# Kernel optimization log

Hardware: AMD Instinct MI355X
Metric: run time of the kernel (lower is better)

## Reference

```python
import jax, jax.numpy as jnp
import numpy as np

# config constants
H = 1024          # hidden_size
I = 512           # moe_intermediate_size
IS = 1024         # moe_shared_expert_intermediate_size
E = 16            # n_routed_experts
G = 4             # n_group
TOPK_G = 2        # topk_group
TOPK = 4          # num_experts_per_tok
SCALE = 2.5       # routed_scaling_factor
B, S = 2, 1024


def _relu2(x):
    r = jax.nn.relu(x)
    return r * r


def setup_inputs() -> dict:
    key = jax.random.key(0)
    ks = jax.random.split(key, 8)
    sd = 0.02
    return {
        "hidden_states": jax.random.normal(ks[0], (B, S, H), jnp.float32),
        "Wg": jax.random.normal(ks[1], (E, H), jnp.float32) * sd,          # router gate weight
        "bias_corr": jax.random.normal(ks[2], (E,), jnp.float32) * 0.01,    # e_score_correction_bias
        "W1": jax.random.normal(ks[3], (E, I, H), jnp.float32) * sd,        # experts up_proj
        "W2": jax.random.normal(ks[4], (E, H, I), jnp.float32) * sd,        # experts down_proj
        "Ws1": jax.random.normal(ks[5], (IS, H), jnp.float32) * sd,         # shared up_proj
        "Ws2": jax.random.normal(ks[6], (H, IS), jnp.float32) * sd,         # shared down_proj
    }


def _route(scores, bias_corr):
    # scores: (T,E) = sigmoid(router logits)
    T = scores.shape[0]
    s_choice = scores + bias_corr                                           # (T,E)
    gs = s_choice.reshape(T, G, E // G)
    group_scores = jnp.sum(jax.lax.top_k(gs, 2)[0], axis=-1)                # (T,G) sum of top-2 per group
    gidx = jax.lax.top_k(group_scores, TOPK_G)[1]                           # (T,topk_group)
    gmask = jnp.sum(jax.nn.one_hot(gidx, G, dtype=scores.dtype), axis=1)    # (T,G)
    smask = jnp.repeat(gmask, E // G, axis=1)                               # (T,E)
    masked = jnp.where(smask > 0, s_choice, 0.0)
    topk_idx = jax.lax.top_k(masked, TOPK)[1]                               # (T,top_k)
    topk_w = jnp.take_along_axis(scores, topk_idx, axis=1)                  # weights from raw sigmoid scores
    topk_w = topk_w / (jnp.sum(topk_w, axis=-1, keepdims=True) + 1e-20)     # norm_topk_prob
    topk_w = topk_w * SCALE
    return topk_idx, topk_w


def reference(hidden_states, Wg, bias_corr, W1, W2, Ws1, Ws2):
    b, s, h = hidden_states.shape
    flat = hidden_states.reshape(-1, h)                                     # (T,H)
    T = flat.shape[0]
    logits = flat.astype(jnp.float32) @ Wg.T                                # (T,E)
    scores = jax.nn.sigmoid(logits)
    topk_idx, topk_w = _route(scores, bias_corr)
    topk_w = topk_w.astype(hidden_states.dtype)
    # combined per-(token, expert) weight; zero where not routed (equivalent
    # to the per-expert gather/MLP/weighted index_add in the original)
    cw = jnp.zeros((T, E), flat.dtype)
    cw = cw.at[jnp.arange(T)[:, None], topk_idx].add(topk_w)                # (T,E)
    # fc1_latent_proj / fc2_latent_proj are Identity (moe_latent_size=None)
    hid = _relu2(jnp.einsum('th,eih->eti', flat, W1))                       # (E,T,I)
    y = jnp.einsum('eti,ehi->eth', hid, W2)                                 # (E,T,H)
    out = jnp.einsum('eth,te->th', y, cw)                                   # (T,H)
    shared = _relu2(flat @ Ws1.T) @ Ws2.T                                   # shared expert on residuals
    return (out + shared).reshape(b, s, h)
```

## Files before the change

### kernel.cpp

```cpp
#include <hip/hip_runtime.h>
#include <hip/hip_bf16.h>

#define T_TOK 2048
#define HDIM 1024
#define IDIM 512
#define ISDIM 1024
#define NEXP 16
#define TOPK 4
#define NSLOT (T_TOK*TOPK)
#define SCALE_F 2.5f

typedef unsigned short u16;
typedef float f32x4 __attribute__((ext_vector_type(4)));
typedef __bf16 bf16x8 __attribute__((ext_vector_type(8)));
typedef u16 u16x8 __attribute__((ext_vector_type(8)));

__device__ __forceinline__ u16 f2bf(float f) {
  unsigned u = __builtin_bit_cast(unsigned, f);
  u += 0x7fffu + ((u >> 16) & 1u);
  return (u16)(u >> 16);
}

__device__ __forceinline__ float bf2f(u16 h) {
  unsigned u = ((unsigned)h) << 16;
  return __builtin_bit_cast(float, u);
}

__device__ __forceinline__ void gload_lds16(const u16* g, u16* l) {
  __builtin_amdgcn_global_load_lds(
      (const __attribute__((address_space(1))) void*)g,
      (__attribute__((address_space(3))) void*)l, 16, 0, 0);
}

__device__ __forceinline__ f32x4 mfma16(u16x8 a, u16x8 b, f32x4 c) {
  return __builtin_amdgcn_mfma_f32_16x16x32_bf16(
      __builtin_bit_cast(bf16x8, a), __builtin_bit_cast(bf16x8, b), c, 0, 0, 0);
}

__device__ __forceinline__ void wait_vm6()   { asm volatile("s_waitcnt vmcnt(6)" ::: "memory"); }
__device__ __forceinline__ void wait_vm0()   { asm volatile("s_waitcnt vmcnt(0)" ::: "memory"); }
__device__ __forceinline__ void wait_lgkm0() { asm volatile("s_waitcnt lgkmcnt(0)" ::: "memory"); }

#define JMAX0 136
#define G0T (8*JMAX0)
#define JMAX1 240
#define G1T (8*JMAX1)
#define MAXG0 96
#define MAXG1 192

#define N1Q (NEXP*IDIM*HDIM/4)
#define N2Q (NEXP*HDIM*IDIM/4)
#define NSQ (ISDIM*HDIM/4)
#define CVTB ((N1Q + NSQ) / 256)

__device__ __forceinline__ void cvt_f4(const float* src, u16* dst, int off) {
  float4 v = reinterpret_cast<const float4*>(src)[off];
  ushort4 o;
  o.x = f2bf(v.x); o.y = f2bf(v.y); o.z = f2bf(v.z); o.w = f2bf(v.w);
  reinterpret_cast<ushort4*>(dst)[off] = o;
}

__global__ void __launch_bounds__(256) router_kernel(
    const float* __restrict__ x, const float* __restrict__ Wg,
    const float* __restrict__ bias,
    int* __restrict__ topk_idx, float* __restrict__ topk_w,
    u16* __restrict__ Xbf,
    int* __restrict__ counts, int* __restrict__ gfill,
    const float* __restrict__ W1, const float* __restrict__ Ws1,
    u16* __restrict__ W1b, u16* __restrict__ Ws1b) {
  int t = blockIdx.x;
  int tid = threadIdx.x;

  if (t >= T_TOK) {
    int i = (t - T_TOK) * 256 + tid;
    if (i < N1Q) cvt_f4(W1, W1b, i);
    else         cvt_f4(Ws1, Ws1b, i - N1Q);
    return;
  }

  int lane = tid & 63;
  int wave = tid >> 6;

  if (t == 0 && tid < NEXP) { counts[tid] = 0; gfill[tid] = 0; }

  __shared__ __align__(16) float sx[HDIM];
  __shared__ float ssc[NEXP];

  float4 xv = reinterpret_cast<const float4*>(x + (size_t)t * HDIM)[tid];
  reinterpret_cast<float4*>(sx)[tid] = xv;
  ushort4 o;
  o.x = f2bf(xv.x); o.y = f2bf(xv.y); o.z = f2bf(xv.z); o.w = f2bf(xv.w);
  reinterpret_cast<ushort4*>(Xbf + (size_t)t * HDIM)[tid] = o;
  __syncthreads();

  float acc[4] = {0.f, 0.f, 0.f, 0.f};
  const float4* sx4 = reinterpret_cast<const float4*>(sx);
#pragma unroll
  for (int c = 0; c < 4; c++) {
    float4 xq = sx4[lane + 64 * c];
#pragma unroll
    for (int e = 0; e < 4; e++) {
      float4 wq = reinterpret_cast<const float4*>(
          Wg + (size_t)(wave * 4 + e) * HDIM)[lane + 64 * c];
      acc[e] += xq.x * wq.x + xq.y * wq.y + xq.z * wq.z + xq.w * wq.w;
    }
  }
#pragma unroll
  for (int e = 0; e < 4; e++) {
    float v = acc[e];
#pragma unroll
    for (int off = 32; off > 0; off >>= 1) v += __shfl_xor(v, off);
    if (lane == 0) ssc[wave * 4 + e] = v;
  }
  __syncthreads();

  if (tid == 0) {
    float scores[NEXP], sc[NEXP];
#pragma unroll
    for (int e = 0; e < NEXP; e++) {
      float s = 1.f / (1.f + expf(-ssc[e]));
      scores[e] = s;
      sc[e] = s + bias[e];
    }
    float gsum[4];
#pragma unroll
    for (int g = 0; g < 4; g++) {
      float a = sc[4*g], b = sc[4*g+1], c = sc[4*g+2], d = sc[4*g+3];
      float hi1 = fmaxf(a, b), lo1 = fminf(a, b);
      float hi2 = fmaxf(c, d), lo2 = fminf(c, d);
      gsum[g] = fmaxf(hi1, hi2) + fmaxf(fminf(hi1, hi2), fmaxf(lo1, lo2));
    }
    int g0 = 0; float bv = gsum[0];
#pragma unroll
    for (int g = 1; g < 4; g++) if (gsum[g] > bv) { bv = gsum[g]; g0 = g; }
    int g1 = -1; float bv2 = -1e30f;
#pragma unroll
    for (int g = 0; g < 4; g++) if (g != g0 && gsum[g] > bv2) { bv2 = gsum[g]; g1 = g; }
    float m[NEXP];
#pragma unroll
    for (int e = 0; e < NEXP; e++) {
      int g = e >> 2;
      m[e] = (g == g0 || g == g1) ? sc[e] : 0.0f;
    }
    int idx[TOPK]; float w[TOPK];
#pragma unroll
    for (int k = 0; k < TOPK; k++) {
      int bj = 0; float bmv = m[0];
#pragma unroll
      for (int j = 1; j < NEXP; j++) if (m[j] > bmv) { bmv = m[j]; bj = j; }
      idx[k] = bj; w[k] = scores[bj];
#pragma unroll
      for (int j = 0; j < NEXP; j++) m[j] = (j == bj) ? -1e30f : m[j];
    }
    float s4 = w[0] + w[1] + w[2] + w[3] + 1e-20f;
    float inv = SCALE_F / s4;
#pragma unroll
    for (int k = 0; k < TOPK; k++) {
      topk_idx[t * TOPK + k] = idx[k];
      topk_w[t * TOPK + k] = w[k] * inv;
    }
  }
}

__global__ void __launch_bounds__(256) hist_kernel(
    const int* __restrict__ topk_idx, int* __restrict__ counts) {
  int j = blockIdx.x * 256 + threadIdx.x;
  int lane = threadIdx.x & 63;
  int e = topk_idx[j];
  unsigned long long m = ~0ull;
#pragma unroll
  for (int b = 0; b < 4; b++) {
    unsigned long long bb = __ballot((e >> b) & 1);
    m &= ((e >> b) & 1) ? bb : ~bb;
  }
  int leader = __ffsll(m) - 1;
  if (lane == leader) atomicAdd(&counts[e], __popcll(m));
}

__global__ void __launch_bounds__(256) scatter_build(
    const int* __restrict__ topk_idx, const float* __restrict__ topk_w,
    const int* __restrict__ counts, int* __restrict__ offsets,
    int* __restrict__ gfill,
    int* __restrict__ perm_token, float* __restrict__ perm_w,
    int* __restrict__ slot_of,
    int* __restrict__ tiles0, int* __restrict__ tiles1) {
  int b = blockIdx.x;
  int tid = threadIdx.x;
  int lane = tid & 63;

  if (b < 32) {
    int c = (lane < NEXP) ? counts[lane] : 0;
    int incl = c;
#pragma unroll
    for (int o = 1; o < 16; o <<= 1) {
      int v = __shfl_up(incl, o);
      if (lane >= o) incl += v;
    }
    int excl = incl - c;

    int j = b * 256 + tid;
    int e = topk_idx[j];
    unsigned long long m = ~0ull;
#pragma unroll
    for (int bb = 0; bb < 4; bb++) {
      unsigned long long bl = __ballot((e >> bb) & 1);
      m &= ((e >> bb) & 1) ? bl : ~bl;
    }
    int leader = __ffsll(m) - 1;
    int rank = __popcll(m & ((1ull << lane) - 1ull));
    int base = 0;
    if (lane == leader) base = atomicAdd(&gfill[e], __popcll(m));
    base = __shfl(base, leader);
    int pos = __shfl(excl, e) + base + rank;
    perm_token[pos] = j >> 2;
    perm_w[pos] = topk_w[j];
    slot_of[j] = pos;
    if (b == 0 && tid < NEXP) offsets[tid] = excl;
    return;
  }

  __shared__ int hcnt[NEXP];
  __shared__ int g0s[MAXG0], g0c[MAXG0], g0n[MAXG0];
  __shared__ int g1s[MAXG1], g1c[MAXG1], g1n[MAXG1];
  __shared__ int sng0, sng1;
  if (tid < NEXP) hcnt[tid] = counts[tid];
  __syncthreads();

  if (tid == 0) {
    int l0=0,l1=0,l2=0,l3=0,l4=0,l5=0,l6=0,l7=0;
    int ng = 0;
#define PLACE0(code0, cn)                                               \
    { int x = 0, lv = l0;                                               \
      if (l1<lv){lv=l1;x=1;} if (l2<lv){lv=l2;x=2;}                     \
      if (l3<lv){lv=l3;x=3;} if (l4<lv){lv=l4;x=4;}                     \
      if (l5<lv){lv=l5;x=5;} if (l6<lv){lv=l6;x=6;}                     \
      if (l7<lv){lv=l7;x=7;}                                            \
      g0s[ng] = x + 8*lv; g0c[ng] = (code0); g0n[ng] = (cn); ng++;      \
      if (x==0)l0+=(cn); else if (x==1)l1+=(cn); else if (x==2)l2+=(cn);\
      else if (x==3)l3+=(cn); else if (x==4)l4+=(cn);                   \
      else if (x==5)l5+=(cn); else if (x==6)l6+=(cn); else l7+=(cn); }
    for (int nb = 0; nb < 8; nb++) PLACE0((16 << 10) | nb, 32);
    for (int e = 0; e < NEXP; e++) {
      int mc = (hcnt[e] + 63) >> 6;
      for (int nb = 0; nb < 4; nb++)
        for (int base = 0; base < mc; base += 32)
          PLACE0((e << 10) | (base << 3) | nb, min(32, mc - base));
    }
    sng0 = ng;
#undef PLACE0
  }
  if (tid == 64) {
    int l0=0,l1=0,l2=0,l3=0,l4=0,l5=0,l6=0,l7=0;
    int ng = 0;
#define PLACE1(code0, cn)                                               \
    { int x = 0, lv = l0;                                               \
      if (l1<lv){lv=l1;x=1;} if (l2<lv){lv=l2;x=2;}                     \
      if (l3<lv){lv=l3;x=3;} if (l4<lv){lv=l4;x=4;}                     \
      if (l5<lv){lv=l5;x=5;} if (l6<lv){lv=l6;x=6;}                     \
      if (l7<lv){lv=l7;x=7;}                                            \
      g1s[ng] = x + 8*lv; g1c[ng] = (code0); g1n[ng] = (cn); ng++;      \
      if (x==0)l0+=(cn); else if (x==1)l1+=(cn); else if (x==2)l2+=(cn);\
      else if (x==3)l3+=(cn); else if (x==4)l4+=(cn);                   \
      else if (x==5)l5+=(cn); else if (x==6)l6+=(cn); else l7+=(cn); }
    for (int eh = 16; eh <= 17; eh++)
      for (int nb = 0; nb < 8; nb++) PLACE1((eh << 10) | nb, 32);
    for (int e = 0; e < NEXP; e++) {
      int mc = (hcnt[e] + 63) >> 6;
      for (int nb = 0; nb < 8; nb++)
        for (int base = 0; base < mc; base += 32)
          PLACE1((e << 10) | (base << 3) | nb, min(32, mc - base));
    }
    sng1 = ng;
#undef PLACE1
  }
  if (tid >= 128) {
    for (int i = tid - 128; i < G0T; i += 128) tiles0[i] = -1;
    for (int i = tid - 128; i < G1T; i += 128) tiles1[i] = -1;
  }
  __syncthreads();

  int ng0 = sng0, ng1 = sng1;
  for (int g = tid; g < ng0; g += 256) {
    int st = g0s[g], c0 = g0c[g], cn = g0n[g];
    for (int mm = 0; mm < cn; mm++) tiles0[st + 8 * mm] = c0 + (mm << 3);
  }
  for (int g = tid; g < ng1; g += 256) {
    int st = g1s[g], c0 = g1c[g], cn = g1n[g];
    for (int mm = 0; mm < cn; mm++) tiles1[st + 8 * mm] = c0 + (mm << 3);
  }
}

#define BM 64
#define BN 128
#define BK 64

template<int PHASE>
__global__ void __launch_bounds__(256) moe_gemm(
    const int* __restrict__ tiles,
    const u16* __restrict__ Xbf, const u16* __restrict__ Hg,
    const u16* __restrict__ Hs,
    const u16* __restrict__ W1b, const u16* __restrict__ W2b,
    const u16* __restrict__ Ws1b, const u16* __restrict__ Ws2b,
    const float* __restrict__ W2f, const float* __restrict__ Ws2f,
    u16* __restrict__ W2bo, u16* __restrict__ Ws2bo,
    const int* __restrict__ eoffs, const int* __restrict__ ecnts,
    const int* __restrict__ rowmap, const float* __restrict__ rowscale,
    u16* __restrict__ HgOut, u16* __restrict__ HsOut,
    u16* __restrict__ Ygb, float* __restrict__ Ys)
{
  constexpr int KL = (PHASE == 0) ? HDIM : IDIM;
  constexpr int NT = KL / BK;

  if (PHASE == 0 && blockIdx.x >= G0T) {
    int i = (blockIdx.x - G0T) * 256 + threadIdx.x;
    if (i < N2Q) cvt_f4(W2f, W2bo, i);
    else         cvt_f4(Ws2f, Ws2bo, i - N2Q);
    return;
  }

  int code = tiles[blockIdx.x];
  if (code < 0) return;
  int e  = code >> 10;
  int mb = (code >> 3) & 127;
  int nb = code & 7;

  bool sh = (e >= NEXP);
  int half = e - NEXP;
  int N, Mloc, rowbase, Astr, Bstr, kb;
  const u16* Abase;
  const u16* Bp;
  if (PHASE == 0) {
    Astr = HDIM; Bstr = HDIM; kb = 0;
    if (sh) { N = ISDIM; Mloc = T_TOK; rowbase = 0; Abase = Xbf; Bp = Ws1b; }
    else    { N = IDIM; Mloc = ecnts[e]; rowbase = eoffs[e]; Abase = Xbf;
              Bp = W1b + (size_t)e * IDIM * HDIM; }
  } else {
    N = HDIM;
    if (sh) { Astr = ISDIM; Bstr = ISDIM; kb = half * IDIM;
              Mloc = T_TOK; rowbase = 0; Abase = Hs; Bp = Ws2b; }
    else    { Astr = IDIM; Bstr = IDIM; kb = 0;
              Mloc = ecnts[e]; rowbase = eoffs[e]; Abase = Hg;
              Bp = W2b + (size_t)e * HDIM * IDIM; }
  }
  int m0 = mb * BM;
  if (m0 >= Mloc) return;
  int n0 = nb * BN;
  if (n0 >= N) return;

  __shared__ __align__(16) u16 sA[2][BM * BK];
  __shared__ __align__(16) u16 sB[2][BN * BK];

  int tid = threadIdx.x;
  int lane = tid & 63;
  int wave = tid >> 6;
  int wm = (wave >> 1) * 32;
  int wn = (wave & 1) * 64;
  int fm = lane & 15;
  int kq = lane >> 4;
  int fsw = fm & 7;

  int lrow8 = lane >> 3;
  int sch = ((lane & 7) ^ lrow8) * 8;

  const u16* AgP[2];
  int aoff[2];
#pragma unroll
  for (int g = 0; g < 2; g++) {
    int rt = 16 * wave + 8 * g + lrow8;
    int ar = m0 + rt;
    int arc = (ar < Mloc) ? ar : (Mloc - 1);
    size_t asrc;
    if (PHASE == 0 && !sh) asrc = (size_t)rowmap[rowbase + arc] * Astr;
    else                   asrc = (size_t)((sh ? 0 : rowbase) + arc) * Astr;
    AgP[g] = Abase + asrc + kb + sch;
    aoff[g] = (16 * wave + 8 * g) * BK;
  }
  const u16* BgP[4];
  int boff[4];
#pragma unroll
  for (int g = 0; g < 4; g++) {
    int rt = 32 * wave + 8 * g + lrow8;
    BgP[g] = Bp + (size_t)(n0 + rt) * Bstr + kb + sch;
    boff[g] = (32 * wave + 8 * g) * BK;
  }

  f32x4 acc[2][4] = {};

#pragma unroll
  for (int g = 0; g < 2; g++) gload_lds16(AgP[g], &sA[0][aoff[g]]);
#pragma unroll
  for (int g = 0; g < 4; g++) gload_lds16(BgP[g], &sB[0][boff[g]]);
#pragma unroll
  for (int g = 0; g < 2; g++) gload_lds16(AgP[g] + BK, &sA[1][aoff[g]]);
#pragma unroll
  for (int g = 0; g < 4; g++) gload_lds16(BgP[g] + BK, &sB[1][boff[g]]);

  for (int t = 0; t < NT - 1; ++t) {
    int cur = t & 1;
    wait_vm6();
    __builtin_amdgcn_s_barrier();
    u16x8 af[2][2], bf[2][4];
#pragma unroll
    for (int ks = 0; ks < 2; ks++) {
      int ch = ((ks * 4 + kq) ^ fsw) * 8;
#pragma unroll
      for (int i = 0; i < 2; i++)
        af[ks][i] = *reinterpret_cast<const u16x8*>(&sA[cur][(wm + 16 * i + fm) * BK + ch]);
#pragma unroll
      for (int j = 0; j < 4; j++)
        bf[ks][j] = *reinterpret_cast<const u16x8*>(&sB[cur][(wn + 16 * j + fm) * BK + ch]);
    }
    wait_lgkm0();
    __builtin_amdgcn_sched_barrier(0);
    __builtin_amdgcn_s_barrier();
    if (t + 2 < NT) {
#pragma unroll
      for (int g = 0; g < 2; g++) gload_lds16(AgP[g] + (t + 2) * BK, &sA[cur][aoff[g]]);
#pragma unroll
      for (int g = 0; g < 4; g++) gload_lds16(BgP[g] + (t + 2) * BK, &sB[cur][boff[g]]);
    }
#pragma unroll
    for (int ks = 0; ks < 2; ks++)
#pragma unroll
      for (int i = 0; i < 2; i++)
#pragma unroll
        for (int j = 0; j < 4; j++)
          acc[i][j] = mfma16(af[ks][i], bf[ks][j], acc[i][j]);
  }
  {
    constexpr int cur = (NT - 1) & 1;
    wait_vm0();
    __builtin_amdgcn_s_barrier();
    u16x8 af[2][2], bf[2][4];
#pragma unroll
    for (int ks = 0; ks < 2; ks++) {
      int ch = ((ks * 4 + kq) ^ fsw) * 8;
#pragma unroll
      for (int i = 0; i < 2; i++)
        af[ks][i] = *reinterpret_cast<const u16x8*>(&sA[cur][(wm + 16 * i + fm) * BK + ch]);
#pragma unroll
      for (int j = 0; j < 4; j++)
        bf[ks][j] = *reinterpret_cast<const u16x8*>(&sB[cur][(wn + 16 * j + fm) * BK + ch]);
    }
    wait_lgkm0();
    __builtin_amdgcn_sched_barrier(0);
#pragma unroll
    for (int ks = 0; ks < 2; ks++)
#pragma unroll
      for (int i = 0; i < 2; i++)
#pragma unroll
        for (int j = 0; j < 4; j++)
          acc[i][j] = mfma16(af[ks][i], bf[ks][j], acc[i][j]);
  }

#pragma unroll
  for (int i = 0; i < 2; i++) {
#pragma unroll
    for (int r = 0; r < 4; r++) {
      int gm = m0 + wm + 16 * i + kq * 4 + r;
      if (gm < Mloc) {
        float rs = 0.f;
        if (PHASE == 0 && !sh) rs = rowscale[rowbase + gm];
#pragma unroll
        for (int j = 0; j < 4; j++) {
          int gn = n0 + wn + 16 * j + fm;
          float v = acc[i][j][r];
          if (PHASE == 0) {
            float tq = fmaxf(v, 0.f);
            if (!sh) {
              tq = tq * tq * rs;
              HgOut[(size_t)(rowbase + gm) * IDIM + gn] = f2bf(tq);
            } else {
              HsOut[(size_t)gm * ISDIM + gn] = f2bf(tq * tq);
            }
          } else {
            if (!sh) Ygb[(size_t)(rowbase + gm) * HDIM + gn] = f2bf(v);
            else     Ys[(size_t)(half * T_TOK + gm) * HDIM + gn] = v;
          }
        }
      }
    }
  }
}

__global__ void __launch_bounds__(256) combine_kernel(
    const u16* __restrict__ Ygb, const float* __restrict__ Ys,
    const int* __restrict__ slot_of, float* __restrict__ out) {
  int t = blockIdx.x;
  int i = threadIdx.x;
  int4 s = *reinterpret_cast<const int4*>(&slot_of[t * 4]);
  const ushort4* Y4 = reinterpret_cast<const ushort4*>(Ygb);
  const float4* S4 = reinterpret_cast<const float4*>(Ys);
  float4* O4 = reinterpret_cast<float4*>(out);
  float4 v0 = S4[(size_t)t * 256 + i];
  float4 v1 = S4[(size_t)(T_TOK + t) * 256 + i];
  ushort4 a = Y4[(size_t)s.x * 256 + i];
  ushort4 b = Y4[(size_t)s.y * 256 + i];
  ushort4 c = Y4[(size_t)s.z * 256 + i];
  ushort4 d = Y4[(size_t)s.w * 256 + i];
  float4 v;
  v.x = v0.x + v1.x + bf2f(a.x) + bf2f(b.x) + bf2f(c.x) + bf2f(d.x);
  v.y = v0.y + v1.y + bf2f(a.y) + bf2f(b.y) + bf2f(c.y) + bf2f(d.y);
  v.z = v0.z + v1.z + bf2f(a.z) + bf2f(b.z) + bf2f(c.z) + bf2f(d.z);
  v.w = v0.w + v1.w + bf2f(a.w) + bf2f(b.w) + bf2f(c.w) + bf2f(d.w);
  O4[(size_t)t * 256 + i] = v;
}

extern "C" void kernel_launch(void* const* d_in, const int* in_sizes, int n_in,
                              void* d_out, int out_size, void* d_ws, size_t ws_size,
                              hipStream_t stream) {
  const float* x    = (const float*)d_in[0];
  const float* Wg   = (const float*)d_in[1];
  const float* bias = (const float*)d_in[2];
  const float* W1   = (const float*)d_in[3];
  const float* W2   = (const float*)d_in[4];
  const float* Ws1  = (const float*)d_in[5];
  const float* Ws2  = (const float*)d_in[6];
  float* out = (float*)d_out;

  char* p = (char*)d_ws;
  auto alloc = [&](size_t bytes) -> void* {
    void* r = (void*)p;
    p += (bytes + 255) & ~(size_t)255;
    return r;
  };
  int*   topk_idx   = (int*)  alloc((size_t)NSLOT * 4);
  float* topk_w     = (float*)alloc((size_t)NSLOT * 4);
  int*   counts     = (int*)  alloc(64);
  int*   offsets    = (int*)  alloc(64);
  int*   gfill      = (int*)  alloc(64);
  int*   perm_token = (int*)  alloc((size_t)NSLOT * 4);
  float* perm_w     = (float*)alloc((size_t)NSLOT * 4);
  int*   slot_of    = (int*)  alloc((size_t)NSLOT * 4);
  int*   tiles0     = (int*)  alloc((size_t)G0T * 4);
  int*   tiles1     = (int*)  alloc((size_t)G1T * 4);
  u16*   Xbf        = (u16*)  alloc((size_t)T_TOK * HDIM * 2);
  u16*   W1b        = (u16*)  alloc((size_t)NEXP * IDIM * HDIM * 2);
  u16*   W2b        = (u16*)  alloc((size_t)NEXP * HDIM * IDIM * 2);
  u16*   Ws1b      = (u16*)  alloc((size_t)ISDIM * HDIM * 2);
  u16*   Ws2b      = (u16*)  alloc((size_t)HDIM * ISDIM * 2);
  u16*   Hg         = (u16*)  alloc((size_t)NSLOT * IDIM * 2);
  u16*   Hs         = (u16*)  alloc((size_t)T_TOK * ISDIM * 2);
  u16*   Ygb        = (u16*)  alloc((size_t)NSLOT * HDIM * 2);
  float* Ys         = (float*)alloc((size_t)2 * T_TOK * HDIM * 4);

  router_kernel<<<T_TOK + CVTB, 256, 0, stream>>>(
      x, Wg, bias, topk_idx, topk_w, Xbf, counts, gfill,
      W1, Ws1, W1b, Ws1b);
  hist_kernel<<<32, 256, 0, stream>>>(topk_idx, counts);
  scatter_build<<<33, 256, 0, stream>>>(topk_idx, topk_w, counts, offsets,
                                        gfill, perm_token, perm_w, slot_of,
                                        tiles0, tiles1);

  moe_gemm<0><<<G0T + CVTB, 256, 0, stream>>>(
      tiles0, Xbf, Hg, Hs, W1b, W2b, Ws1b, Ws2b, W2, Ws2, W2b, Ws2b,
      offsets, counts, perm_token, perm_w, Hg, Hs, nullptr, nullptr);

  moe_gemm<1><<<G1T, 256, 0, stream>>>(
      tiles1, Xbf, Hg, Hs, W1b, W2b, Ws1b, Ws2b, W2, Ws2, W2b, Ws2b,
      offsets, counts, perm_token, perm_w, Hg, Hs, Ygb, Ys);

  combine_kernel<<<T_TOK, 256, 0, stream>>>(Ygb, Ys, slot_of, out);
}
```

Before: 227.5 us.

## Drop split-K shared down-proj, fold histogram into router, store shared output bf16

The shared expert's down-projection no longer runs as two K-halves writing fp32 partial sums. It runs as one full-K tile set writing bf16, so phase 1 has fewer tiles and the combine reads one bf16 buffer instead of two fp32 ones. The separate histogram kernel is removed: the router atomically increments the expert counts, and counts/gfill are cleared with a memset. The changes cut launches and memory traffic, but the shared tiles become longer and may unbalance the schedule, and per-slot atomics add contention.

```diff
diff --git a/kernel.cpp b/kernel.cpp
--- a/kernel.cpp
+++ b/kernel.cpp
@@ -43,7 +43,7 @@
 
 #define JMAX0 136
 #define G0T (8*JMAX0)
-#define JMAX1 240
+#define JMAX1 208
 #define G1T (8*JMAX1)
 #define MAXG0 96
 #define MAXG1 192
@@ -64,8 +64,7 @@
     const float* __restrict__ x, const float* __restrict__ Wg,
     const float* __restrict__ bias,
     int* __restrict__ topk_idx, float* __restrict__ topk_w,
-    u16* __restrict__ Xbf,
-    int* __restrict__ counts, int* __restrict__ gfill,
+    u16* __restrict__ Xbf, int* __restrict__ counts,
     const float* __restrict__ W1, const float* __restrict__ Ws1,
     u16* __restrict__ W1b, u16* __restrict__ Ws1b) {
   int t = blockIdx.x;
@@ -80,8 +79,6 @@
 
   int lane = tid & 63;
   int wave = tid >> 6;
-
-  if (t == 0 && tid < NEXP) { counts[tid] = 0; gfill[tid] = 0; }
 
   __shared__ __align__(16) float sx[HDIM];
   __shared__ float ssc[NEXP];
@@ -158,23 +155,9 @@
     for (int k = 0; k < TOPK; k++) {
       topk_idx[t * TOPK + k] = idx[k];
       topk_w[t * TOPK + k] = w[k] * inv;
-    }
-  }
-}
-
-__global__ void __launch_bounds__(256) hist_kernel(
-    const int* __restrict__ topk_idx, int* __restrict__ counts) {
-  int j = blockIdx.x * 256 + threadIdx.x;
-  int lane = threadIdx.x & 63;
-  int e = topk_idx[j];
-  unsigned long long m = ~0ull;
-#pragma unroll
-  for (int b = 0; b < 4; b++) {
-    unsigned long long bb = __ballot((e >> b) & 1);
-    m &= ((e >> b) & 1) ? bb : ~bb;
-  }
-  int leader = __ffsll(m) - 1;
-  if (lane == leader) atomicAdd(&counts[e], __popcll(m));
+      atomicAdd(&counts[idx[k]], 1);
+    }
+  }
 }
 
 __global__ void __launch_bounds__(256) scatter_build(
@@ -262,8 +245,7 @@
       if (x==0)l0+=(cn); else if (x==1)l1+=(cn); else if (x==2)l2+=(cn);\
       else if (x==3)l3+=(cn); else if (x==4)l4+=(cn);                   \
       else if (x==5)l5+=(cn); else if (x==6)l6+=(cn); else l7+=(cn); }
-    for (int eh = 16; eh <= 17; eh++)
-      for (int nb = 0; nb < 8; nb++) PLACE1((eh << 10) | nb, 32);
+    for (int nb = 0; nb < 8; nb++) PLACE1((16 << 10) | nb, 32);
     for (int e = 0; e < NEXP; e++) {
       int mc = (hcnt[e] + 63) >> 6;
       for (int nb = 0; nb < 8; nb++)
@@ -306,11 +288,8 @@
     const int* __restrict__ eoffs, const int* __restrict__ ecnts,
     const int* __restrict__ rowmap, const float* __restrict__ rowscale,
     u16* __restrict__ HgOut, u16* __restrict__ HsOut,
-    u16* __restrict__ Ygb, float* __restrict__ Ys)
+    u16* __restrict__ Ygb, u16* __restrict__ Ysb)
 {
-  constexpr int KL = (PHASE == 0) ? HDIM : IDIM;
-  constexpr int NT = KL / BK;
-
   if (PHASE == 0 && blockIdx.x >= G0T) {
     int i = (blockIdx.x - G0T) * 256 + threadIdx.x;
     if (i < N2Q) cvt_f4(W2f, W2bo, i);
@@ -325,20 +304,20 @@
   int nb = code & 7;
 
   bool sh = (e >= NEXP);
-  int half = e - NEXP;
-  int N, Mloc, rowbase, Astr, Bstr, kb;
+  int N, Mloc, rowbase, Astr, Bstr;
+  int NT;
   const u16* Abase;
   const u16* Bp;
   if (PHASE == 0) {
-    Astr = HDIM; Bstr = HDIM; kb = 0;
+    Astr = HDIM; Bstr = HDIM; NT = HDIM / BK;
     if (sh) { N = ISDIM; Mloc = T_TOK; rowbase = 0; Abase = Xbf; Bp = Ws1b; }
     else    { N = IDIM; Mloc = ecnts[e]; rowbase = eoffs[e]; Abase = Xbf;
               Bp = W1b + (size_t)e * IDIM * HDIM; }
   } else {
     N = HDIM;
-    if (sh) { Astr = ISDIM; Bstr = ISDIM; kb = half * IDIM;
+    if (sh) { Astr = ISDIM; Bstr = ISDIM; NT = ISDIM / BK;
               Mloc = T_TOK; rowbase = 0; Abase = Hs; Bp = Ws2b; }
-    else    { Astr = IDIM; Bstr = IDIM; kb = 0;
+    else    { Astr = IDIM; Bstr = IDIM; NT = IDIM / BK;
               Mloc = ecnts[e]; rowbase = eoffs[e]; Abase = Hg;
               Bp = W2b + (size_t)e * HDIM * IDIM; }
   }
@@ -372,7 +351,7 @@
     size_t asrc;
     if (PHASE == 0 && !sh) asrc = (size_t)rowmap[rowbase + arc] * Astr;
     else                   asrc = (size_t)((sh ? 0 : rowbase) + arc) * Astr;
-    AgP[g] = Abase + asrc + kb + sch;
+    AgP[g] = Abase + asrc + sch;
     aoff[g] = (16 * wave + 8 * g) * BK;
   }
   const u16* BgP[4];
@@ -380,7 +359,7 @@
 #pragma unroll
   for (int g = 0; g < 4; g++) {
     int rt = 32 * wave + 8 * g + lrow8;
-    BgP[g] = Bp + (size_t)(n0 + rt) * Bstr + kb + sch;
+    BgP[g] = Bp + (size_t)(n0 + rt) * Bstr + sch;
     boff[g] = (32 * wave + 8 * g) * BK;
   }
 
@@ -428,7 +407,7 @@
           acc[i][j] = mfma16(af[ks][i], bf[ks][j], acc[i][j]);
   }
   {
-    constexpr int cur = (NT - 1) & 1;
+    int cur = (NT - 1) & 1;
     wait_vm0();
     __builtin_amdgcn_s_barrier();
     u16x8 af[2][2], bf[2][4];
@@ -475,7 +454,7 @@
             }
           } else {
             if (!sh) Ygb[(size_t)(rowbase + gm) * HDIM + gn] = f2bf(v);
-            else     Ys[(size_t)(half * T_TOK + gm) * HDIM + gn] = v;
+            else     Ysb[(size_t)gm * HDIM + gn] = f2bf(v);
           }
         }
       }
@@ -484,25 +463,24 @@
 }
 
 __global__ void __launch_bounds__(256) combine_kernel(
-    const u16* __restrict__ Ygb, const float* __restrict__ Ys,
+    const u16* __restrict__ Ygb, const u16* __restrict__ Ysb,
     const int* __restrict__ slot_of, float* __restrict__ out) {
   int t = blockIdx.x;
   int i = threadIdx.x;
   int4 s = *reinterpret_cast<const int4*>(&slot_of[t * 4]);
   const ushort4* Y4 = reinterpret_cast<const ushort4*>(Ygb);
-  const float4* S4 = reinterpret_cast<const float4*>(Ys);
+  const ushort4* S4 = reinterpret_cast<const ushort4*>(Ysb);
   float4* O4 = reinterpret_cast<float4*>(out);
-  float4 v0 = S4[(size_t)t * 256 + i];
-  float4 v1 = S4[(size_t)(T_TOK + t) * 256 + i];
+  ushort4 sv = S4[(size_t)t * 256 + i];
   ushort4 a = Y4[(size_t)s.x * 256 + i];
   ushort4 b = Y4[(size_t)s.y * 256 + i];
   ushort4 c = Y4[(size_t)s.z * 256 + i];
   ushort4 d = Y4[(size_t)s.w * 256 + i];
   float4 v;
-  v.x = v0.x + v1.x + bf2f(a.x) + bf2f(b.x) + bf2f(c.x) + bf2f(d.x);
-  v.y = v0.y + v1.y + bf2f(a.y) + bf2f(b.y) + bf2f(c.y) + bf2f(d.y);
-  v.z = v0.z + v1.z + bf2f(a.z) + bf2f(b.z) + bf2f(c.z) + bf2f(d.z);
-  v.w = v0.w + v1.w + bf2f(a.w) + bf2f(b.w) + bf2f(c.w) + bf2f(d.w);
+  v.x = bf2f(sv.x) + bf2f(a.x) + bf2f(b.x) + bf2f(c.x) + bf2f(d.x);
+  v.y = bf2f(sv.y) + bf2f(a.y) + bf2f(b.y) + bf2f(c.y) + bf2f(d.y);
+  v.z = bf2f(sv.z) + bf2f(a.z) + bf2f(b.z) + bf2f(c.z) + bf2f(d.z);
+  v.w = bf2f(sv.w) + bf2f(a.w) + bf2f(b.w) + bf2f(c.w) + bf2f(d.w);
   O4[(size_t)t * 256 + i] = v;
 }
 
@@ -542,12 +520,12 @@
   u16*   Hg         = (u16*)  alloc((size_t)NSLOT * IDIM * 2);
   u16*   Hs         = (u16*)  alloc((size_t)T_TOK * ISDIM * 2);
   u16*   Ygb        = (u16*)  alloc((size_t)NSLOT * HDIM * 2);
-  float* Ys         = (float*)alloc((size_t)2 * T_TOK * HDIM * 4);
+  u16*   Ysb        = (u16*)  alloc((size_t)T_TOK * HDIM * 2);
+
+  hipMemsetAsync(counts, 0, 768, stream);
 
   router_kernel<<<T_TOK + CVTB, 256, 0, stream>>>(
-      x, Wg, bias, topk_idx, topk_w, Xbf, counts, gfill,
-      W1, Ws1, W1b, Ws1b);
-  hist_kernel<<<32, 256, 0, stream>>>(topk_idx, counts);
+      x, Wg, bias, topk_idx, topk_w, Xbf, counts, W1, Ws1, W1b, Ws1b);
   scatter_build<<<33, 256, 0, stream>>>(topk_idx, topk_w, counts, offsets,
                                         gfill, perm_token, perm_w, slot_of,
                                         tiles0, tiles1);
@@ -558,7 +536,7 @@
 
   moe_gemm<1><<<G1T, 256, 0, stream>>>(
       tiles1, Xbf, Hg, Hs, W1b, W2b, Ws1b, Ws2b, W2, Ws2, W2b, Ws2b,
-      offsets, counts, perm_token, perm_w, Hg, Hs, Ygb, Ys);
-
-  combine_kernel<<<T_TOK, 256, 0, stream>>>(Ygb, Ys, slot_of, out);
-}
+      offsets, counts, perm_token, perm_w, Hg, Hs, Ygb, Ysb);
+
+  combine_kernel<<<T_TOK, 256, 0, stream>>>(Ygb, Ysb, slot_of, out);
+}
```

Result: slower. 302.2 us (+32.9%).
